# Optimization experiments

Measured on AMD Instinct MI355X. Metric: run time of the kernel, lower is better.

Reference implementation:

```python
import jax, jax.numpy as jnp
import numpy as np
from jax.scipy.special import i0

B, P = 2, 524288
N = (512, 512)            # uniform frequency grid
M = 4                     # window cutoff m (2M taps per dim)
SIGMA = 2.0
NGRID = tuple(2 * (int(SIGMA * Ni) // 2) for Ni in N)  # oversampled grid (1024, 1024)
BETA = tuple(float(np.pi * (2.0 - 1.0 / (ng / Ni))) for ng, Ni in zip(NGRID, N))


def _phi_hat_1d(Ni, ni, b):
    # Fourier coefficients of the Kaiser-Bessel window, k = -Ni/2 .. Ni/2-1
    k = jnp.arange(-Ni // 2, Ni // 2, dtype=jnp.float32)
    arg = jnp.sqrt(b * b - (2.0 * jnp.pi * k / ni) ** 2)
    return i0(M * arg) / ni


def _window_ft():
    # separable d-dim Fourier coefficient grid, shape [N1, N2] (== window.ft)
    c1 = _phi_hat_1d(N[0], NGRID[0], BETA[0])
    c2 = _phi_hat_1d(N[1], NGRID[1], BETA[1])
    return c1[:, None] * c2[None, :]


def _phi(t, ni, b):
    # Kaiser-Bessel window in time domain, support |t| <= M/ni
    u2 = M * M - (ni * t) ** 2
    u = jnp.sqrt(jnp.maximum(u2, 1e-12))
    return jnp.where(u2 > 0, jnp.sinh(b * u) / (jnp.pi * u), 0.0)


def setup_inputs() -> dict:
    key = jax.random.key(0)
    k1, k2 = jax.random.split(key)
    x = jax.random.uniform(k1, (B, P, 2), jnp.float32, -0.5, 0.5)  # points on torus
    f_hat = jax.random.normal(k2, (B, N[0], N[1], 2), jnp.float32)  # complex as [re,im]
    return {"x": x, "f_hat": f_hat}


def _nfft_forward(x, f_hat):
    # f(x_j) ~= sum_k f_hat[k] exp(-2 pi i <k, x_j>) via window-deconvolved oversampled FFT + local gather
    fh = (f_hat[..., 0] + 1j * f_hat[..., 1]).astype(jnp.complex64)  # [B, N1, N2]
    ft = _window_ft().astype(jnp.float32)
    gh = fh / ft                                                    # deconvolve
    p1 = (NGRID[0] - N[0]) // 2
    p2 = (NGRID[1] - N[1]) // 2
    gh = jnp.pad(gh, ((0, 0), (p1, p1), (p2, p2)))                  # centered zero-pad to n
    g = jnp.fft.fftn(jnp.fft.ifftshift(gh, axes=(-2, -1)), axes=(-2, -1))
    g = g / (NGRID[0] * NGRID[1])                                   # g_l = (1/n) sum_k gh_k e^{-2pi i kl/n}

    offs = jnp.arange(-M + 1, M + 1)                                # [2M]
    ws, idxs = [], []
    for d in range(2):
        nd = NGRID[d]
        xd = x[..., d]                                              # [B, P]
        l0 = jnp.floor(xd * nd).astype(jnp.int32)
        l = l0[..., None] + offs                                    # [B, P, 2M]
        t = xd[..., None] - l.astype(jnp.float32) / nd
        ws.append(_phi(t, nd, BETA[d]))
        idxs.append(jnp.mod(l, nd))

    g_flat = g.reshape(B, NGRID[0] * NGRID[1])
    acc = jnp.zeros((B, P), jnp.complex64)
    for i in range(2 * M):                                          # fixed 2m x 2m taps
        for j in range(2 * M):
            flat = idxs[0][..., i] * NGRID[1] + idxs[1][..., j]     # [B, P]
            gv = jnp.take_along_axis(g_flat, flat, axis=1)
            acc = acc + (ws[0][..., i] * ws[1][..., j]) * gv
    return jnp.stack([acc.real, acc.imag], axis=-1)                 # [B, P, 2]


def reference(x, f_hat):
    return _nfft_forward(x, f_hat)
```

## Files before the change

kernel.cpp:

```cpp
#include <hip/hip_runtime.h>

constexpr int   NGRID = 1024;
constexpr int   BATCH = 2;
constexpr int   NPTS  = 524288;
constexpr int   BINS  = 2048;
constexpr int   CAP   = 768;
constexpr float BETA  = 4.71238898038469f;
constexpr float PI_F  = 3.14159265358979f;

#define PIDX(i) ((i) + ((i) >> 4))

constexpr size_t G_BYTES  = (size_t)BATCH * NGRID * NGRID * sizeof(float2);
constexpr size_t GCNT_OFF = G_BYTES;
constexpr size_t PERM_OFF = G_BYTES + 8192;

__device__ __forceinline__ float i0f_large(float x) {
    float t = 3.75f / x;
    float p =  0.00392377f;
    p = p * t + -0.01647633f;
    p = p * t +  0.02635537f;
    p = p * t + -0.02057706f;
    p = p * t +  0.00916281f;
    p = p * t + -0.00157565f;
    p = p * t +  0.00225319f;
    p = p * t +  0.01328592f;
    p = p * t +  0.39894228f;
    return __expf(x) * rsqrtf(x) * p;
}

__device__ __forceinline__ int tile_of(float2 xv, int b) {
    int c1 = ((int)floorf(xv.x * 1024.0f)) & 1023;
    int c2 = ((int)floorf(xv.y * 1024.0f)) & 1023;
    return (b << 10) + ((c1 >> 5) << 5) + (c2 >> 5);
}

__device__ __forceinline__ float2 cmul(float2 a, float2 w) {
    return make_float2(a.x * w.x - a.y * w.y, a.x * w.y + a.y * w.x);
}

__device__ __forceinline__ int digitrev4_10(int f) {
    unsigned r = __brev((unsigned)f) >> 22;
    return (int)(((r & 0x2AAu) >> 1) | ((r & 0x155u) << 1));
}

__device__ __forceinline__ void build_tw4(float2* T, int tid, int nthreads) {
    int off = 0, q = 256, sig = 1;
    #pragma unroll
    for (int st = 0; st < 5; ++st) {
        for (int m = tid; m < 3 * q; m += nthreads) {
            int sec = 0, j = m;
            if (j >= q) { sec++; j -= q; }
            if (j >= q) { sec++; j -= q; }
            float ang = (-2.0f * PI_F / 1024.0f) * (float)((sec + 1) * j * sig);
            float sw, cw;
            __sincosf(ang, &sw, &cw);
            T[off + m] = make_float2(cw, sw);
        }
        off += 3 * q; q >>= 2; sig <<= 2;
    }
}

__device__ __forceinline__ void bfly4(float2* s, const float2* T,
                                      int bt, int q, int off) {
    int j    = bt & (q - 1);
    int base = ((bt - j) << 2) + j;
    int p0 = PIDX(base), p1 = PIDX(base + q);
    int p2 = PIDX(base + 2 * q), p3 = PIDX(base + 3 * q);
    float2 a0 = s[p0], a1 = s[p1], a2 = s[p2], a3 = s[p3];
    float2 t0 = make_float2(a0.x + a2.x, a0.y + a2.y);
    float2 t1 = make_float2(a0.x - a2.x, a0.y - a2.y);
    float2 t2 = make_float2(a1.x + a3.x, a1.y + a3.y);
    float2 t3 = make_float2(a1.x - a3.x, a1.y - a3.y);
    float2 b0 = make_float2(t0.x + t2.x, t0.y + t2.y);
    float2 b2 = make_float2(t0.x - t2.x, t0.y - t2.y);
    float2 b1 = make_float2(t1.x + t3.y, t1.y - t3.x);
    float2 b3 = make_float2(t1.x - t3.y, t1.y + t3.x);
    s[p0] = b0;
    s[p1] = cmul(b1, T[off + j]);
    s[p2] = cmul(b2, T[off + q + j]);
    s[p3] = cmul(b3, T[off + 2 * q + j]);
}

__global__ __launch_bounds__(256) void rows_and_bin(const float2* __restrict__ fh,
                                                    float2* __restrict__ g,
                                                    const float2* __restrict__ x,
                                                    int* __restrict__ gcnt,
                                                    int* __restrict__ perm) {
    __shared__ __align__(16) char smem[16880];
    int tid = threadIdx.x;

    if (blockIdx.x < 1024) {
        float2* s = (float2*)smem;
        float2* T = (float2*)smem + 1087;
        int blk = blockIdx.x & 511;
        int b   = blockIdx.x >> 9;
        int row = (blk < 256) ? blk : blk + 512;
        int a1  = (row + 256) & 1023;

        build_tw4(T, tid, 256);

        float k1 = (float)(a1 - 256);
        float w1 = (2.0f * PI_F / 1024.0f) * k1;
        float c1 = i0f_large(4.0f * sqrtf(BETA * BETA - w1 * w1));

        const float2* fr = fh + ((long)b << 18) + ((long)a1 << 9);

        float w2a = (2.0f * PI_F / 1024.0f) * (float)tid;
        float c2a = i0f_large(4.0f * sqrtf(BETA * BETA - w2a * w2a));
        float w2b = (2.0f * PI_F / 1024.0f) * (float)(tid - 256);
        float c2b = i0f_large(4.0f * sqrtf(BETA * BETA - w2b * w2b));

        float2 va = fr[tid + 256];
        float2 vb = fr[tid];
        float ia = 1.0f / (c1 * c2a);
        float ib = 1.0f / (c1 * c2b);
        s[PIDX(tid)]       = make_float2(va.x * ia, va.y * ia);
        s[PIDX(tid + 256)] = make_float2(0.f, 0.f);
        s[PIDX(tid + 512)] = make_float2(0.f, 0.f);
        s[PIDX(tid + 768)] = make_float2(vb.x * ib, vb.y * ib);

        int off = 0, q = 256;
        #pragma unroll
        for (int st = 0; st < 5; ++st) {
            __syncthreads();
            bfly4(s, T, tid, q, off);
            off += 3 * q; q >>= 2;
        }
        __syncthreads();

        float2* base = g + ((long)b << 20) + ((long)row << 10);
        #pragma unroll
        for (int i = 0; i < 4; ++i) {
            int idx = tid + (i << 8);
            base[idx] = s[PIDX(digitrev4_10(idx))];
        }
    } else {
        int* h = (int*)smem;
        int bblk = blockIdx.x - 1024;
        for (int i = tid; i < BINS; i += 256) h[i] = 0;
        __syncthreads();

        int base = bblk * 4096;
        int tile[16];
        #pragma unroll
        for (int i = 0; i < 16; ++i) {
            int gid = base + tid + i * 256;
            tile[i] = tile_of(x[gid], gid >> 19);
            atomicAdd(&h[tile[i]], 1);
        }
        __syncthreads();

        #pragma unroll
        for (int j = 0; j < 8; ++j) {
            int bi = tid + j * 256;
            int c  = h[bi];
            h[bi]  = c ? atomicAdd(&gcnt[bi], c) : 0;
        }
        __syncthreads();

        #pragma unroll
        for (int i = 0; i < 16; ++i) {
            int pos = atomicAdd(&h[tile[i]], 1);
            perm[tile[i] * CAP + pos] = base + tid + i * 256;
        }
    }
}

__global__ __launch_bounds__(256) void fft_cols(float2* __restrict__ g) {
    constexpr int STR = 1092;
    __shared__ float2 s[4 * STR];
    __shared__ float2 T[1023];
    int b  = blockIdx.y;
    int C0 = blockIdx.x * 4;
    int t  = threadIdx.x;
    int c  = t & 3, L = t >> 2;
    float2* gb = g + ((long)b << 20);

    build_tw4(T, t, 256);

    float2* sf = s + c * STR;
    #pragma unroll
    for (int i = 0; i < 4; ++i) {
        int r = L + i * 64;
        sf[PIDX(r)] = gb[((long)r << 10) + C0 + c];
    }
    #pragma unroll
    for (int i = 0; i < 4; ++i) {
        int r = L + i * 64 + 768;
        sf[PIDX(r)] = gb[((long)r << 10) + C0 + c];
    }
    #pragma unroll
    for (int i = 0; i < 8; ++i) {
        int r = L + i * 64 + 256;
        sf[PIDX(r)] = make_float2(0.f, 0.f);
    }

    int off = 0, q = 256;
    #pragma unroll
    for (int st = 0; st < 5; ++st) {
        __syncthreads();
        #pragma unroll
        for (int rr = 0; rr < 4; ++rr)
            bfly4(sf, T, L + rr * 64, q, off);
        off += 3 * q; q >>= 2;
    }
    __syncthreads();

    #pragma unroll
    for (int i = 0; i < 16; ++i) {
        int r = L + i * 64;
        gb[((long)r << 10) + C0 + c] = sf[PIDX(digitrev4_10(r))];
    }
}

__global__ __launch_bounds__(256) void gather_binned(const float2* __restrict__ x,
                                                     const float2* __restrict__ g,
                                                     const int* __restrict__ gcnt,
                                                     const int* __restrict__ perm,
                                                     float2* __restrict__ out) {
    __shared__ float2 patch[37 * 37];
    int tb = blockIdx.x;
    int b  = tb >> 10;
    int tt = tb & 1023;
    int tR = tt >> 5, tC = tt & 31;
    int R0 = (tR << 5) - 2, C0 = (tC << 5) - 2;
    const float2* gb = g + ((long)b << 20);

    for (int p = threadIdx.x; p < 37 * 37; p += 256) {
        int pr = p / 37, pc = p - pr * 37;
        int gr = (R0 + pr) & 1023, gc = (C0 + pc) & 1023;
        patch[p] = gb[(gr << 10) + gc];
    }
    __syncthreads();

    int cnt = gcnt[tb];
    if (cnt > CAP) cnt = CAP;
    int off0 = tb * CAP;
    for (int i = (int)threadIdx.x; i < cnt; i += 256) {
        int gid = perm[off0 + i];
        float2 xv = x[gid];

        float w1[6], w2[6];
        int rr0, cc0;
        {
            float xs = xv.x * 1024.0f;
            float fl = floorf(xs);
            float fr = xs - fl;
            rr0 = (((int)fl) & 1023) - (tR << 5);
            #pragma unroll
            for (int k = 0; k < 6; ++k) {
                float tv = fr - (float)(k - 2);
                float u2 = 16.0f - tv * tv;
                float ir = rsqrtf(u2);
                float z  = BETA * u2 * ir;
                w1[k] = __expf(z) * 0.159154943f * ir;
            }
        }
        {
            float xs = xv.y * 1024.0f;
            float fl = floorf(xs);
            float fr = xs - fl;
            cc0 = (((int)fl) & 1023) - (tC << 5);
            #pragma unroll
            for (int k = 0; k < 6; ++k) {
                float tv = fr - (float)(k - 2);
                float u2 = 16.0f - tv * tv;
                float ir = rsqrtf(u2);
                float z  = BETA * u2 * ir;
                w2[k] = __expf(z) * 0.159154943f * ir;
            }
        }

        float ar = 0.0f, ai = 0.0f;
        #pragma unroll
        for (int ii = 0; ii < 6; ++ii) {
            int pbase = (rr0 + ii) * 37 + cc0;
            float wi = w1[ii];
            #pragma unroll
            for (int jj = 0; jj < 6; ++jj) {
                float2 gv = patch[pbase + jj];
                float w = wi * w2[jj];
                ar = fmaf(w, gv.x, ar);
                ai = fmaf(w, gv.y, ai);
            }
        }
        out[gid] = make_float2(ar, ai);
    }
}

extern "C" void kernel_launch(void* const* d_in, const int* in_sizes, int n_in,
                              void* d_out, int out_size, void* d_ws, size_t ws_size,
                              hipStream_t stream) {
    const float2* x  = (const float2*)d_in[0];
    const float2* fh = (const float2*)d_in[1];
    char* ws = (char*)d_ws;
    float2* g   = (float2*)ws;
    int* gcnt   = (int*)(ws + GCNT_OFF);
    int* perm   = (int*)(ws + PERM_OFF);

    hipMemsetAsync(gcnt, 0, BINS * sizeof(int), stream);

    rows_and_bin<<<dim3(1280), dim3(256), 0, stream>>>(fh, g, x, gcnt, perm);
    fft_cols    <<<dim3(256, BATCH), dim3(256), 0, stream>>>(g);

    gather_binned<<<dim3(BINS), dim3(256), 0, stream>>>(x, g, gcnt, perm, (float2*)d_out);
}
```

Baseline: 123.6 us.

## Prune zero-padded FFT first stages and tabulate window weights in shared memory

The row FFT now computes its first radix-4 stage in registers, exploiting that only two of the four input quarters are non-zero, and skips zero-filling shared memory. The column FFT loads only the non-zero rows into registers and does the first two radix-4 stages there before writing to shared memory, leaving three shared-memory stages. The gather kernel replaces per-point exp/rsqrt window evaluation with a 128-entry-per-tap linear interpolation table built in shared memory. The table adds interpolation error compared with exact evaluation, and the extra register arrays may raise register pressure.

After: 128.1 us. 1.04x slower.

```diff
diff --git a/kernel.cpp b/kernel.cpp
--- a/kernel.cpp
+++ b/kernel.cpp
@@ -114,14 +114,19 @@
         float2 vb = fr[tid];
         float ia = 1.0f / (c1 * c2a);
         float ib = 1.0f / (c1 * c2b);
-        s[PIDX(tid)]       = make_float2(va.x * ia, va.y * ia);
-        s[PIDX(tid + 256)] = make_float2(0.f, 0.f);
-        s[PIDX(tid + 512)] = make_float2(0.f, 0.f);
-        s[PIDX(tid + 768)] = make_float2(vb.x * ib, vb.y * ib);
-
-        int off = 0, q = 256;
-        #pragma unroll
-        for (int st = 0; st < 5; ++st) {
+        float2 A = make_float2(va.x * ia, va.y * ia);
+        float2 B = make_float2(vb.x * ib, vb.y * ib);
+
+        __syncthreads();
+
+        s[PIDX(tid)]       = make_float2(A.x + B.x, A.y + B.y);
+        s[PIDX(tid + 256)] = cmul(make_float2(A.x - B.y, A.y + B.x), T[tid]);
+        s[PIDX(tid + 512)] = cmul(make_float2(A.x - B.x, A.y - B.y), T[256 + tid]);
+        s[PIDX(tid + 768)] = cmul(make_float2(A.x + B.y, A.y - B.x), T[512 + tid]);
+
+        int off = 768, q = 64;
+        #pragma unroll
+        for (int st = 0; st < 4; ++st) {
             __syncthreads();
             bfly4(s, T, tid, q, off);
             off += 3 * q; q >>= 2;
@@ -178,26 +183,52 @@
 
     build_tw4(T, t, 256);
 
+    float2 E[16];
+    #pragma unroll
+    for (int m = 0; m < 4; ++m) {
+        int r = L + 64 * m;
+        E[m] = gb[((long)r << 10) + C0 + c];
+    }
+    #pragma unroll
+    for (int m = 12; m < 16; ++m) {
+        int r = L + 64 * m;
+        E[m] = gb[((long)r << 10) + C0 + c];
+    }
+    __syncthreads();
+
+    #pragma unroll
+    for (int m = 0; m < 4; ++m) {
+        float2 A = E[m], B = E[m + 12];
+        int j = L + 64 * m;
+        E[m]      = make_float2(A.x + B.x, A.y + B.y);
+        E[m + 4]  = cmul(make_float2(A.x - B.y, A.y + B.x), T[j]);
+        E[m + 8]  = cmul(make_float2(A.x - B.x, A.y - B.y), T[256 + j]);
+        E[m + 12] = cmul(make_float2(A.x + B.y, A.y - B.x), T[512 + j]);
+    }
+
+    {
+        float2 u1 = T[768 + L], u2 = T[768 + 64 + L], u3 = T[768 + 128 + L];
+        #pragma unroll
+        for (int a = 0; a < 4; ++a) {
+            float2 a0 = E[4*a], a1 = E[4*a+1], a2 = E[4*a+2], a3 = E[4*a+3];
+            float2 t0 = make_float2(a0.x + a2.x, a0.y + a2.y);
+            float2 t1 = make_float2(a0.x - a2.x, a0.y - a2.y);
+            float2 t2 = make_float2(a1.x + a3.x, a1.y + a3.y);
+            float2 t3 = make_float2(a1.x - a3.x, a1.y - a3.y);
+            E[4*a]   = make_float2(t0.x + t2.x, t0.y + t2.y);
+            E[4*a+1] = cmul(make_float2(t1.x + t3.y, t1.y - t3.x), u1);
+            E[4*a+2] = cmul(make_float2(t0.x - t2.x, t0.y - t2.y), u2);
+            E[4*a+3] = cmul(make_float2(t1.x - t3.y, t1.y + t3.x), u3);
+        }
+    }
+
     float2* sf = s + c * STR;
     #pragma unroll
-    for (int i = 0; i < 4; ++i) {
-        int r = L + i * 64;
-        sf[PIDX(r)] = gb[((long)r << 10) + C0 + c];
-    }
-    #pragma unroll
-    for (int i = 0; i < 4; ++i) {
-        int r = L + i * 64 + 768;
-        sf[PIDX(r)] = gb[((long)r << 10) + C0 + c];
-    }
-    #pragma unroll
-    for (int i = 0; i < 8; ++i) {
-        int r = L + i * 64 + 256;
-        sf[PIDX(r)] = make_float2(0.f, 0.f);
-    }
-
-    int off = 0, q = 256;
-    #pragma unroll
-    for (int st = 0; st < 5; ++st) {
+    for (int m = 0; m < 16; ++m) sf[PIDX(L + 64 * m)] = E[m];
+
+    int off = 960, q = 16;
+    #pragma unroll
+    for (int st = 0; st < 3; ++st) {
         __syncthreads();
         #pragma unroll
         for (int rr = 0; rr < 4; ++rr)
@@ -219,6 +250,7 @@
                                                      const int* __restrict__ perm,
                                                      float2* __restrict__ out) {
     __shared__ float2 patch[37 * 37];
+    __shared__ float2 W[6 * 128];
     int tb = blockIdx.x;
     int b  = tb >> 10;
     int tt = tb & 1023;
@@ -230,6 +262,16 @@
         int pr = p / 37, pc = p - pr * 37;
         int gr = (R0 + pr) & 1023, gc = (C0 + pc) & 1023;
         patch[p] = gb[(gr << 10) + gc];
+    }
+    for (int e = threadIdx.x; e < 768; e += 256) {
+        int k = e >> 7, i = e & 127;
+        float t0 = (float)i * 0.0078125f - (float)(k - 2);
+        float t1 = t0 + 0.0078125f;
+        float u20 = 16.0f - t0 * t0, u21 = 16.0f - t1 * t1;
+        float ir0 = rsqrtf(u20),     ir1 = rsqrtf(u21);
+        float v0 = __expf(BETA * u20 * ir0) * 0.159154943f * ir0;
+        float v1 = __expf(BETA * u21 * ir1) * 0.159154943f * ir1;
+        W[e] = make_float2(v0, v1 - v0);
     }
     __syncthreads();
 
@@ -247,13 +289,13 @@
             float fl = floorf(xs);
             float fr = xs - fl;
             rr0 = (((int)fl) & 1023) - (tR << 5);
+            float fi = fr * 128.0f;
+            int   ti = (int)fi;
+            float fc = fi - (float)ti;
             #pragma unroll
             for (int k = 0; k < 6; ++k) {
-                float tv = fr - (float)(k - 2);
-                float u2 = 16.0f - tv * tv;
-                float ir = rsqrtf(u2);
-                float z  = BETA * u2 * ir;
-                w1[k] = __expf(z) * 0.159154943f * ir;
+                float2 wd = W[(k << 7) + ti];
+                w1[k] = fmaf(fc, wd.y, wd.x);
             }
         }
         {
@@ -261,13 +303,13 @@
             float fl = floorf(xs);
             float fr = xs - fl;
             cc0 = (((int)fl) & 1023) - (tC << 5);
+            float fi = fr * 128.0f;
+            int   ti = (int)fi;
+            float fc = fi - (float)ti;
             #pragma unroll
             for (int k = 0; k < 6; ++k) {
-                float tv = fr - (float)(k - 2);
-                float u2 = 16.0f - tv * tv;
-                float ir = rsqrtf(u2);
-                float z  = BETA * u2 * ir;
-                w2[k] = __expf(z) * 0.159154943f * ir;
+                float2 wd = W[(k << 7) + ti];
+                w2[k] = fmaf(fc, wd.y, wd.x);
             }
         }
 
```
